# Kernel optimization log

Measured on AMD Instinct MI355X. Metric: run time of the kernel, lower is better.

Reference implementation:

```python
import jax, jax.numpy as jnp
import numpy as np

N = 100000   # num_nodes
E = 1600000  # num_edges
H = 128      # hidden_dim
OUT = 1      # output_dim
SLOPE = 0.2  # GATConv leaky_relu negative_slope


def setup_inputs() -> dict:
    key = jax.random.key(0)
    ks = jax.random.split(key, 10)
    s = 1.0 / np.sqrt(H)
    return {
        "h": jnp.arange(N, dtype=jnp.int64 if jax.config.jax_enable_x64 else jnp.int32),
        "edge_index": jax.random.randint(ks[0], (2, E), 0, N),
        "node_type": jax.random.randint(ks[1], (N,), 0, 3),
        "emb": jax.random.normal(ks[2], (N, H), jnp.float32) * s,
        "W1": jax.random.normal(ks[3], (H, H), jnp.float32) * s,
        "a_src1": jax.random.normal(ks[4], (H,), jnp.float32) * s,
        "a_dst1": jax.random.normal(ks[5], (H,), jnp.float32) * s,
        "b1": jnp.zeros((H,), jnp.float32),
        "W2": jax.random.normal(ks[6], (H, OUT), jnp.float32) * s,
        "a_src2": jax.random.normal(ks[7], (OUT,), jnp.float32) * s,
        "a_dst2": jax.random.normal(ks[8], (OUT,), jnp.float32) * s,
        "b2": jnp.zeros((OUT,), jnp.float32),
    }


def gat_layer(x, src, dst, emask, W, a_src, a_dst, b, n_nodes):
    """PyG GATConv (heads=1, add_self_loops=True). Masked edges get -inf logits."""
    xp = x @ W                                  # [N, F]
    e_src = xp @ a_src                          # [N]
    e_dst = xp @ a_dst                          # [N]
    logits = jax.nn.leaky_relu(e_src[src] + e_dst[dst], SLOPE)   # [E]
    logits = jnp.where(emask, logits, -jnp.inf)
    self_logits = jax.nn.leaky_relu(e_src + e_dst, SLOPE)        # [N] self-loops
    # segment softmax over destination nodes (edges + self loop)
    m = jax.ops.segment_max(logits, dst, num_segments=n_nodes)
    m = jnp.maximum(m, self_logits)             # finite: self loop always present
    ew = jnp.exp(logits - m[dst])               # masked edges -> exp(-inf)=0
    sw = jnp.exp(self_logits - m)
    denom = jax.ops.segment_sum(ew, dst, num_segments=n_nodes) + sw
    alpha = ew / denom[dst]                     # [E]
    alpha_self = sw / denom                     # [N]
    out = jax.ops.segment_sum(alpha[:, None] * xp[src], dst, num_segments=n_nodes)
    out = out + alpha_self[:, None] * xp + b
    return out


def reference(h, edge_index, node_type, emb, W1, a_src1, a_dst1, b1, W2, a_src2, a_dst2, b2):
    src, dst = edge_index[0], edge_index[1]
    emask = (node_type[src] == 0) & (node_type[dst] == 0)
    x = emb[h]                                          # embedding lookup [N, H]
    x = gat_layer(x, src, dst, emask, W1, a_src1, a_dst1, b1, emb.shape[0])
    x = jax.nn.relu(x)
    x = gat_layer(x, src, dst, emask, W2, a_src2, a_dst2, b2, emb.shape[0])
    return x
```

## Files before the change

kernel.cpp:

```cpp
#include <hip/hip_runtime.h>

#define N_NODES 100000
#define N_EDGES 1600000
#define HD 128
#define SLOPE 0.2f
#define NBLK 391
#define GB 782
#define EB2 3125
#define CAP 32

typedef __attribute__((ext_vector_type(8))) short bf16x8;
typedef __attribute__((ext_vector_type(4))) float f32x4;

__device__ __forceinline__ unsigned short f2bf(float f) {
    union { float f; unsigned u; } v; v.f = f;
    const unsigned u = v.u + 0x7FFFu + ((v.u >> 16) & 1u);
    return (unsigned short)(u >> 16);
}
__device__ __forceinline__ unsigned pack2(float lo, float hi) {
    return (unsigned)f2bf(lo) | ((unsigned)f2bf(hi) << 16);
}
__device__ __forceinline__ float bf2f(unsigned u16) {
    union { unsigned u; float f; } v; v.u = u16 << 16; return v.f;
}

__global__ __launch_bounds__(256) void k0_zero(
    const int* __restrict__ nt, const float* __restrict__ W1,
    int* __restrict__ deg, unsigned* __restrict__ umask,
    unsigned short* __restrict__ W1bfT)
{
    const int i = blockIdx.x * 256 + threadIdx.x;
    bool act = false;
    if (i < N_NODES) { deg[i] = 0; act = (nt[i] == 0); }
    const unsigned long long bal = __ballot(act);
    const int lane = threadIdx.x & 63;
    if (lane == 0)       umask[i >> 5] = (unsigned)bal;
    else if (lane == 32) umask[i >> 5] = (unsigned)(bal >> 32);
    if (i < HD * HD) {
        const int n = i >> 7, k = i & 127;
        W1bfT[n * HD + k] = f2bf(W1[k * HD + n]);
    }
}

__global__ __launch_bounds__(512, 8) void k1_gemm_edge(
    const int* __restrict__ h,
    const float* __restrict__ emb,
    const unsigned short* __restrict__ W1bfT,
    const float* __restrict__ a_src1,
    const float* __restrict__ a_dst1,
    unsigned short* __restrict__ xp1,
    float* __restrict__ es1,
    float* __restrict__ ed1,
    float* __restrict__ denom1,
    const int* __restrict__ ei,
    const unsigned* __restrict__ umask,
    int* __restrict__ deg,
    int* __restrict__ adj)
{
    __shared__ unsigned short Wlds[HD * HD];
    const int tid = threadIdx.x;

    if (blockIdx.x < EB2) {
        const int e = blockIdx.x * 512 + tid;
        const int src = ei[e];
        const int dst = ei[N_EDGES + e];
        const bool active =
            (((umask[src >> 5] >> (src & 31)) & (umask[dst >> 5] >> (dst & 31))) & 1u) != 0u;
        if (active) {
            const int slot = atomicAdd(deg + dst, 1);
            if (slot < CAP) adj[(size_t)dst * CAP + slot] = src;
        }
        return;
    }
    const int vb = blockIdx.x - EB2;

    {
        const int n  = tid >> 2;
        const int kq = (tid & 3) * 32;
        const unsigned short* src = W1bfT + n * HD + kq;
        #pragma unroll
        for (int j = 0; j < 4; ++j) {
            const int c = (kq >> 3) + j;
            const int p = c ^ (n & 7);
            *(bf16x8*)(Wlds + n * HD + p * 8) = *(const bf16x8*)(src + j * 8);
        }
    }

    const int w   = tid >> 6;
    const int L   = tid & 63;
    const int lm  = L & 15;
    const int lg  = L >> 4;
    const int wrow0 = vb * 128 + w * 16;

    const int arow = wrow0 + lm;
    const int g = (arow < N_NODES) ? arow : (N_NODES - 1);
    const float* xrow = emb + (size_t)h[g] * HD;

    __syncthreads();

    f32x4 acc[8];
    #pragma unroll
    for (int ct = 0; ct < 8; ++ct) acc[ct] = (f32x4)0.f;

    #pragma unroll
    for (int ks = 0; ks < 4; ++ks) {
        const int k0 = ks * 32 + lg * 8;
        const float4 u = *(const float4*)(xrow + k0);
        const float4 v = *(const float4*)(xrow + k0 + 4);
        union { bf16x8 b; unsigned x[4]; } t;
        t.x[0] = pack2(u.x, u.y);
        t.x[1] = pack2(u.z, u.w);
        t.x[2] = pack2(v.x, v.y);
        t.x[3] = pack2(v.z, v.w);
        const bf16x8 af = t.b;

        const int c = k0 >> 3;
        const int p = (c ^ (lm & 7)) * 8;
        #pragma unroll
        for (int ct = 0; ct < 8; ++ct) {
            const bf16x8 bfr = *(const bf16x8*)(Wlds + (ct * 16 + lm) * HD + p);
            acc[ct] = __builtin_amdgcn_mfma_f32_16x16x32_bf16(af, bfr, acc[ct], 0, 0, 0);
        }
    }

    float asv[8], adv[8];
    #pragma unroll
    for (int ct = 0; ct < 8; ++ct) {
        asv[ct] = a_src1[ct * 16 + lm];
        adv[ct] = a_dst1[ct * 16 + lm];
    }

    #pragma unroll
    for (int reg = 0; reg < 4; ++reg) {
        const int row = wrow0 + lg * 4 + reg;
        float s = 0.f, d = 0.f;
        #pragma unroll
        for (int ct = 0; ct < 8; ++ct) {
            s += acc[ct][reg] * asv[ct];
            d += acc[ct][reg] * adv[ct];
        }
        #pragma unroll
        for (int m = 1; m < 16; m <<= 1) {
            s += __shfl_xor(s, m, 64);
            d += __shfl_xor(d, m, 64);
        }
        if (row < N_NODES) {
            unsigned short* dst = xp1 + (size_t)row * HD;
            #pragma unroll
            for (int ct = 0; ct < 8; ++ct)
                dst[ct * 16 + lm] = f2bf(acc[ct][reg]);
            if (lm == 0) {
                const float sum = s + d;
                const float l = sum > 0.f ? sum : SLOPE * sum;
                es1[row] = s;
                ed1[row] = d;
                denom1[row] = __expf(l);
            }
        }
    }
}

__global__ __launch_bounds__(256) void k2_gather(
    const unsigned short* __restrict__ xp1, const float* __restrict__ denom1,
    const float* __restrict__ es1, const float* __restrict__ ed1,
    const int* __restrict__ deg, const int* __restrict__ adj,
    const float* __restrict__ b1, const float* __restrict__ W2,
    float* __restrict__ xp2)
{
    const int wid = threadIdx.x >> 6;
    const int lane = threadIdx.x & 63;
    const int i = blockIdx.x * 4 + wid;
    if (i >= N_NODES) return;

    const int dcount = min(deg[i], CAP);

    const unsigned pself = ((const unsigned*)(xp1 + (size_t)i * HD))[lane];
    float a0 = bf2f(pself & 0xFFFFu);
    float a1 = bf2f(pself >> 16);

    if (dcount > 0) {
        const float wself = denom1[i];
        const float edv   = ed1[i];
        const int* arow = adj + (size_t)i * CAP;

        int nidx = 0; float nw = 0.f;
        if (lane < dcount) {
            nidx = arow[lane];
            const float lgt = es1[nidx] + edv;
            nw = __expf(lgt > 0.f ? lgt : SLOPE * lgt);
        }
        float dsum = nw;
        #pragma unroll
        for (int m = 32; m > 0; m >>= 1) dsum += __shfl_xor(dsum, m, 64);
        const float inv = 1.f / (wself + dsum);

        a0 *= wself;
        a1 *= wself;

        int j = 0;
        for (; j + 2 <= dcount; j += 2) {
            const int   s0 = __shfl(nidx, j, 64);
            const int   s1 = __shfl(nidx, j + 1, 64);
            const float w0 = __shfl(nw, j, 64);
            const float w1 = __shfl(nw, j + 1, 64);
            const unsigned p0 = ((const unsigned*)(xp1 + (size_t)s0 * HD))[lane];
            const unsigned p1 = ((const unsigned*)(xp1 + (size_t)s1 * HD))[lane];
            a0 += w0 * bf2f(p0 & 0xFFFFu) + w1 * bf2f(p1 & 0xFFFFu);
            a1 += w0 * bf2f(p0 >> 16)     + w1 * bf2f(p1 >> 16);
        }
        if (j < dcount) {
            const int   s0 = __shfl(nidx, j, 64);
            const float w0 = __shfl(nw, j, 64);
            const unsigned p0 = ((const unsigned*)(xp1 + (size_t)s0 * HD))[lane];
            a0 += w0 * bf2f(p0 & 0xFFFFu);
            a1 += w0 * bf2f(p0 >> 16);
        }
        a0 *= inv;
        a1 *= inv;
    }

    const float o0 = fmaxf(a0 + b1[2 * lane],     0.f);
    const float o1 = fmaxf(a1 + b1[2 * lane + 1], 0.f);

    float part = o0 * W2[2 * lane] + o1 * W2[2 * lane + 1];
    #pragma unroll
    for (int off = 32; off > 0; off >>= 1) part += __shfl_down(part, off, 64);
    if (lane == 0) xp2[i] = part;
}

__global__ __launch_bounds__(256) void k3_final(
    const float* __restrict__ xp2, const int* __restrict__ deg,
    const int* __restrict__ adj,
    const float* __restrict__ a_src2, const float* __restrict__ a_dst2,
    const float* __restrict__ b2, float* __restrict__ out)
{
    const int i = blockIdx.x * 256 + threadIdx.x;
    if (i >= N_NODES) return;

    const float xi = xp2[i];
    const int dcount = min(deg[i], CAP);
    if (dcount == 0) {
        out[i] = xi + b2[0];
        return;
    }

    const float as = a_src2[0], ad = a_dst2[0];
    const float adxi = ad * xi;
    const float s0 = (as + ad) * xi;
    const float l0 = s0 > 0.f ? s0 : SLOPE * s0;
    const float wself = __expf(l0);

    float denom = wself, num = wself * xi;
    const int* arow = adj + (size_t)i * CAP;

    int j = 0;
    for (; j + 2 <= dcount; j += 2) {
        const int2 ss = *(const int2*)(arow + j);
        const float x0 = xp2[ss.x];
        const float x1 = xp2[ss.y];
        float l0e = as * x0 + adxi; l0e = l0e > 0.f ? l0e : SLOPE * l0e;
        float l1e = as * x1 + adxi; l1e = l1e > 0.f ? l1e : SLOPE * l1e;
        const float w0 = __expf(l0e);
        const float w1 = __expf(l1e);
        denom += w0 + w1;
        num   += w0 * x0 + w1 * x1;
    }
    if (j < dcount) {
        const float x0 = xp2[arow[j]];
        float l0e = as * x0 + adxi; l0e = l0e > 0.f ? l0e : SLOPE * l0e;
        const float w0 = __expf(l0e);
        denom += w0;
        num   += w0 * x0;
    }
    out[i] = num / denom + b2[0];
}

extern "C" void kernel_launch(void* const* d_in, const int* in_sizes, int n_in,
                              void* d_out, int out_size, void* d_ws, size_t ws_size,
                              hipStream_t stream)
{
    const int* h   = (const int*)d_in[0];
    const int* ei  = (const int*)d_in[1];
    const int* nt  = (const int*)d_in[2];
    const float* emb    = (const float*)d_in[3];
    const float* W1     = (const float*)d_in[4];
    const float* a_src1 = (const float*)d_in[5];
    const float* a_dst1 = (const float*)d_in[6];
    const float* b1     = (const float*)d_in[7];
    const float* W2     = (const float*)d_in[8];
    const float* a_src2 = (const float*)d_in[9];
    const float* a_dst2 = (const float*)d_in[10];
    const float* b2     = (const float*)d_in[11];
    float* out = (float*)d_out;

    char* ws = (char*)d_ws;
    size_t off = 0;
    unsigned short* xp1 = (unsigned short*)(ws + off); off += (size_t)N_NODES * HD * sizeof(unsigned short);
    float* es1    = (float*)(ws + off); off += (size_t)N_NODES * sizeof(float);
    float* ed1    = (float*)(ws + off); off += (size_t)N_NODES * sizeof(float);
    float* denom1 = (float*)(ws + off); off += (size_t)N_NODES * sizeof(float);
    float* xp2    = (float*)(ws + off); off += (size_t)N_NODES * sizeof(float);
    int*   deg    = (int*)(ws + off);   off += (size_t)N_NODES * sizeof(int);
    unsigned* umask = (unsigned*)(ws + off); off += 3200 * sizeof(unsigned);
    unsigned short* W1bfT = (unsigned short*)(ws + off); off += (size_t)HD * HD * sizeof(unsigned short);
    off = (off + 255) & ~(size_t)255;
    int*   adj    = (int*)(ws + off);   off += (size_t)N_NODES * CAP * sizeof(int);

    k0_zero<<<NBLK, 256, 0, stream>>>(nt, W1, deg, umask, W1bfT);
    k1_gemm_edge<<<EB2 + GB, 512, 0, stream>>>(
        h, emb, W1bfT, a_src1, a_dst1, xp1, es1, ed1, denom1,
        ei, umask, deg, adj);
    k2_gather<<<(N_NODES + 3) / 4, 256, 0, stream>>>(
        xp1, denom1, es1, ed1, deg, adj, b1, W2, xp2);
    k3_final<<<NBLK, 256, 0, stream>>>(
        xp2, deg, adj, a_src2, a_dst2, b2, out);
}
```

Before: 180.5 us.

## Split edge-bucketing from GEMM kernel and stage GEMM output through LDS

Splits the fused edge/GEMM kernel into two launches: an edge-bucketing kernel that handles two edges per thread with int2 loads, and a GEMM kernel. The GEMM kernel now reuses the weight LDS buffer (padded row stride) to transpose its bf16 accumulators, so each row is written to global memory with 16-byte vector stores instead of scattered 2-byte stores. This targets uncoalesced store traffic and the per-thread edge overhead. In exchange it adds an extra kernel launch, loses the overlap between edge and GEMM blocks that the fused grid gave, and adds two block barriers.

```diff
diff --git a/kernel.cpp b/kernel.cpp
--- a/kernel.cpp
+++ b/kernel.cpp
@@ -6,8 +6,9 @@
 #define SLOPE 0.2f
 #define NBLK 391
 #define GB 782
-#define EB2 3125
+#define EB3 1563
 #define CAP 32
+#define SLICE_LD 136
 
 typedef __attribute__((ext_vector_type(8))) short bf16x8;
 typedef __attribute__((ext_vector_type(4))) float f32x4;
@@ -42,7 +43,30 @@
     }
 }
 
-__global__ __launch_bounds__(512, 8) void k1_gemm_edge(
+__global__ __launch_bounds__(512) void k1a_edge(
+    const int* __restrict__ ei, const unsigned* __restrict__ umask,
+    int* __restrict__ deg, int* __restrict__ adj)
+{
+    const int t = blockIdx.x * 512 + threadIdx.x;
+    const int e0 = t * 2;
+    if (e0 >= N_EDGES) return;
+    const int2 s2 = *(const int2*)(ei + e0);
+    const int2 d2 = *(const int2*)(ei + N_EDGES + e0);
+    const bool a0 =
+        (((umask[s2.x >> 5] >> (s2.x & 31)) & (umask[d2.x >> 5] >> (d2.x & 31))) & 1u) != 0u;
+    const bool a1 =
+        (((umask[s2.y >> 5] >> (s2.y & 31)) & (umask[d2.y >> 5] >> (d2.y & 31))) & 1u) != 0u;
+    if (a0) {
+        const int sl = atomicAdd(deg + d2.x, 1);
+        if (sl < CAP) adj[(size_t)d2.x * CAP + sl] = s2.x;
+    }
+    if (a1) {
+        const int sl = atomicAdd(deg + d2.y, 1);
+        if (sl < CAP) adj[(size_t)d2.y * CAP + sl] = s2.y;
+    }
+}
+
+__global__ __launch_bounds__(512, 8) void k1b_gemm(
     const int* __restrict__ h,
     const float* __restrict__ emb,
     const unsigned short* __restrict__ W1bfT,
@@ -51,28 +75,10 @@
     unsigned short* __restrict__ xp1,
     float* __restrict__ es1,
     float* __restrict__ ed1,
-    float* __restrict__ denom1,
-    const int* __restrict__ ei,
-    const unsigned* __restrict__ umask,
-    int* __restrict__ deg,
-    int* __restrict__ adj)
-{
-    __shared__ unsigned short Wlds[HD * HD];
+    float* __restrict__ denom1)
+{
+    __shared__ unsigned short Wlds[8 * 16 * SLICE_LD];
     const int tid = threadIdx.x;
-
-    if (blockIdx.x < EB2) {
-        const int e = blockIdx.x * 512 + tid;
-        const int src = ei[e];
-        const int dst = ei[N_EDGES + e];
-        const bool active =
-            (((umask[src >> 5] >> (src & 31)) & (umask[dst >> 5] >> (dst & 31))) & 1u) != 0u;
-        if (active) {
-            const int slot = atomicAdd(deg + dst, 1);
-            if (slot < CAP) adj[(size_t)dst * CAP + slot] = src;
-        }
-        return;
-    }
-    const int vb = blockIdx.x - EB2;
 
     {
         const int n  = tid >> 2;
@@ -90,7 +96,7 @@
     const int L   = tid & 63;
     const int lm  = L & 15;
     const int lg  = L >> 4;
-    const int wrow0 = vb * 128 + w * 16;
+    const int wrow0 = blockIdx.x * 128 + w * 16;
 
     const int arow = wrow0 + lm;
     const int g = (arow < N_NODES) ? arow : (N_NODES - 1);
@@ -144,18 +150,30 @@
             s += __shfl_xor(s, m, 64);
             d += __shfl_xor(d, m, 64);
         }
+        if (row < N_NODES && lm == 0) {
+            const float sum = s + d;
+            const float l = sum > 0.f ? sum : SLOPE * sum;
+            es1[row] = s;
+            ed1[row] = d;
+            denom1[row] = __expf(l);
+        }
+    }
+
+    __syncthreads();
+    unsigned short* slice = Wlds + w * 16 * SLICE_LD;
+    #pragma unroll
+    for (int ct = 0; ct < 8; ++ct)
+        #pragma unroll
+        for (int reg = 0; reg < 4; ++reg)
+            slice[(lg * 4 + reg) * SLICE_LD + ct * 16 + lm] = f2bf(acc[ct][reg]);
+    __syncthreads();
+    #pragma unroll
+    for (int rr = 0; rr < 4; ++rr) {
+        const int rl = rr * 4 + lg;
+        const int row = wrow0 + rl;
         if (row < N_NODES) {
-            unsigned short* dst = xp1 + (size_t)row * HD;
-            #pragma unroll
-            for (int ct = 0; ct < 8; ++ct)
-                dst[ct * 16 + lm] = f2bf(acc[ct][reg]);
-            if (lm == 0) {
-                const float sum = s + d;
-                const float l = sum > 0.f ? sum : SLOPE * sum;
-                es1[row] = s;
-                ed1[row] = d;
-                denom1[row] = __expf(l);
-            }
+            const bf16x8 vdat = *(const bf16x8*)(slice + rl * SLICE_LD + lm * 8);
+            *(bf16x8*)(xp1 + (size_t)row * HD + lm * 8) = vdat;
         }
     }
 }
@@ -307,9 +325,9 @@
     int*   adj    = (int*)(ws + off);   off += (size_t)N_NODES * CAP * sizeof(int);
 
     k0_zero<<<NBLK, 256, 0, stream>>>(nt, W1, deg, umask, W1bfT);
-    k1_gemm_edge<<<EB2 + GB, 512, 0, stream>>>(
-        h, emb, W1bfT, a_src1, a_dst1, xp1, es1, ed1, denom1,
-        ei, umask, deg, adj);
+    k1a_edge<<<EB3, 512, 0, stream>>>(ei, umask, deg, adj);
+    k1b_gemm<<<GB, 512, 0, stream>>>(
+        h, emb, W1bfT, a_src1, a_dst1, xp1, es1, ed1, denom1);
     k2_gather<<<(N_NODES + 3) / 4, 256, 0, stream>>>(
         xp1, denom1, es1, ed1, deg, adj, b1, W2, xp2);
     k3_final<<<NBLK, 256, 0, stream>>>(
```

Result: no change. 178.2 us (-1.3%).
